# Kernel optimization log

Measured on AMD Instinct MI355X. Metric: run time of the kernel, lower is better.

The kernel has to match this reference:

```python
import jax, jax.numpy as jnp
import numpy as np

N, E, C, H, G, NC = 100000, 1600000, 128, 128, 256, 10
NEG_SLOPE = 0.2


def setup_inputs() -> dict:
    key = jax.random.key(0)
    ks = jax.random.split(key, 12)
    return {
        "x": jax.random.normal(ks[0], (N, C), jnp.float32),
        "edge_index": jax.random.randint(ks[1], (2, E), 0, N),
        "edge_attr": jax.random.uniform(ks[2], (E,), jnp.float32),
        "batch": jnp.sort(jax.random.randint(ks[3], (N,), 0, G)),
        "num_graphs": G,
        "att": jax.random.normal(ks[4], (3, 2 * C), jnp.float32) * (6.0 / (1 + 2 * C)) ** 0.5,
        "W1": jax.random.normal(ks[5], (3, C, H), jnp.float32) * (1.0 / C) ** 0.5,
        "b1": jnp.zeros((3, H), jnp.float32),
        "W2": jax.random.normal(ks[6], (3, H, H), jnp.float32) * (1.0 / H) ** 0.5,
        "b2": jnp.zeros((3, H), jnp.float32),
        "fc1_w": jax.random.normal(ks[7], (6 * H, 2 * H), jnp.float32) * (1.0 / (6 * H)) ** 0.5,
        "fc1_b": jnp.zeros((2 * H,), jnp.float32),
        "fc2_w": jax.random.normal(ks[8], (2 * H, H), jnp.float32) * (1.0 / (2 * H)) ** 0.5,
        "fc2_b": jnp.zeros((H,), jnp.float32),
        "fc3_w": jax.random.normal(ks[9], (H, NC), jnp.float32) * (1.0 / H) ** 0.5,
        "fc3_b": jnp.zeros((NC,), jnp.float32),
    }


def segment_sparsemax(z, seg, num_segments):
    """Exact sparsemax within each segment (ragged), vectorized via lexsort."""
    n = z.shape[0]
    order = jnp.lexsort((-z, seg))          # by segment asc, value desc
    zs, ss = z[order], seg[order]
    counts = jax.ops.segment_sum(jnp.ones((n,), jnp.int32), seg, num_segments)
    starts = jnp.cumsum(counts) - counts    # exclusive prefix -> segment start
    pos = jnp.arange(n, dtype=jnp.int32) - starts[ss]   # 0-based rank in segment
    ecs = jnp.cumsum(zs)
    base = jnp.concatenate([jnp.zeros((1,), zs.dtype), ecs])[starts[ss]]
    segcum = ecs - base                     # inclusive within-segment cumsum
    cond = 1.0 + (pos + 1).astype(zs.dtype) * zs > segcum  # support prefix mask
    k = jax.ops.segment_sum(cond.astype(zs.dtype), ss, num_segments)
    sum_k = jax.ops.segment_sum(jnp.where(cond, zs, 0.0), ss, num_segments)
    tau = jnp.where(k > 0, (sum_k - 1.0) / jnp.maximum(k, 1.0), 0.0)
    return jnp.maximum(z - tau[seg], 0.0)


def gcn_conv(x, row, col, ew, W, b, n_nodes):
    """PyG GCNConv with edge weights + self-loops (fill value 1)."""
    h = x @ W                                            # [N, H]
    deg = jax.ops.segment_sum(ew, col, n_nodes) + 1.0    # self-loop weight 1
    dinv = jnp.where(deg > 0, jax.lax.rsqrt(deg), 0.0)
    norm = dinv[row] * ew * dinv[col]                    # per-edge norm
    out = jax.ops.segment_sum(norm[:, None] * h[row], col, n_nodes)
    out = out + h * (dinv * dinv)[:, None]               # self-loop contribution
    return out + b


def emodel_block(x, row, col, att_b, W1_b, b1_b, W2_b, b2_b, n_nodes):
    # Edgelayer: att * cat([x[row], x[col]]) summed -> leaky_relu -> sparsemax(row)
    c = x.shape[1]
    s1 = x @ att_b[:c]                                   # [N]
    s2 = x @ att_b[c:]
    w = s1[row] + s2[col]
    w = jnp.where(w >= 0, w, NEG_SLOPE * w)              # leaky_relu
    p = segment_sparsemax(w, row, n_nodes)               # zero weight == pruned edge
    h = jax.nn.relu(gcn_conv(x, row, col, p, W1_b, b1_b, n_nodes))
    h = jax.nn.relu(gcn_conv(h, row, col, p, W2_b, b2_b, n_nodes))
    return h


def global_pools(z, batch, num_graphs):
    cnt = jax.ops.segment_sum(jnp.ones((z.shape[0], 1), z.dtype), batch, num_graphs)
    mean = jax.ops.segment_sum(z, batch, num_graphs) / jnp.maximum(cnt, 1.0)
    mx = jax.ops.segment_max(z, batch, num_graphs)
    mx = jnp.where(jnp.isfinite(mx), mx, 0.0)            # guard empty graphs
    return mean, mx


def reference(x, edge_index, edge_attr, batch, num_graphs, att, W1, b1, W2, b2,
              fc1_w, fc1_b, fc2_w, fc2_b, fc3_w, fc3_b):
    n_nodes = x.shape[0]
    row, col = edge_index[0], edge_index[1]
    feats = []
    for i in range(3):  # three structurally identical blocks with distinct params
        z = emodel_block(x, row, col, att[i], W1[i], b1[i], W2[i], b2[i], n_nodes)
        mean, mx = global_pools(z, batch, num_graphs)
        feats += [mean, mx]
    h = jnp.concatenate(feats, axis=1)                   # [G, 6*H]
    h = jax.nn.relu(h @ fc1_w + fc1_b)
    h = jax.nn.relu(h @ fc2_w + fc2_b)
    return jax.nn.log_softmax(h @ fc3_w + fc3_b, axis=-1)
```

## Files before the change

kernel.cpp:

```cpp
#include <hip/hip_runtime.h>
#include <math.h>

constexpr int NN   = 100000;
constexpr int EE   = 1600000;
constexpr int CH   = 128;
constexpr int GG   = 256;
constexpr int NCLS = 10;
constexpr int SW   = 48;
constexpr int QW   = 24;

constexpr int NB   = (NN + 63) >> 6;
constexpr int BCAP = 1344;
constexpr int EPT  = 8;
constexpr int BINTB = 256;
constexpr int EPB  = BINTB * EPT;

typedef _Float16 half8  __attribute__((ext_vector_type(8)));
typedef _Float16 half2v __attribute__((ext_vector_type(2)));
typedef float    float4v __attribute__((ext_vector_type(4)));

__global__ void bounds_kernel(const int* __restrict__ batch, int* __restrict__ gb,
                              int* __restrict__ bcur) {
    int t = blockIdx.x * blockDim.x + threadIdx.x;
    if (t < NB) bcur[t] = 0;
    if (t > GG) return;
    int lo = 0, hi = NN;
    while (lo < hi) {
        int mid = (lo + hi) >> 1;
        if (batch[mid] < t) lo = mid + 1; else hi = mid;
    }
    gb[t] = lo;
}

__global__ void wt16_kernel(const float* __restrict__ W1, const float* __restrict__ W2,
                            _Float16* __restrict__ wt) {
    int mat = blockIdx.x;
    const float* src = (mat < 3) ? (W1 + (size_t)mat * 16384)
                                 : (W2 + (size_t)(mat - 3) * 16384);
    _Float16* dst = wt + (size_t)mat * 16384;
    for (int i = threadIdx.x; i < 16384; i += 256) {
        int n = i >> 7, k = i & 127;
        dst[n * 128 + k] = (_Float16)src[k * 128 + n];
    }
}

__global__ void scores3_kernel(const float* __restrict__ x, const float* __restrict__ att,
                               float* __restrict__ s1, float* __restrict__ s2,
                               int* __restrict__ cur, _Float16* __restrict__ x16) {
    int wid  = threadIdx.x >> 6;
    int lane = threadIdx.x & 63;
    int node = blockIdx.x * 4 + wid;
    if (node >= NN) return;
    float x0 = x[node * CH + lane];
    float x1 = x[node * CH + 64 + lane];
    x16[(size_t)node * CH + lane]      = (_Float16)x0;
    x16[(size_t)node * CH + 64 + lane] = (_Float16)x1;
#pragma unroll
    for (int i = 0; i < 3; ++i) {
        const float* a = att + i * 256;
        float p1 = x0 * a[lane]       + x1 * a[64 + lane];
        float p2 = x0 * a[128 + lane] + x1 * a[192 + lane];
#pragma unroll
        for (int off = 32; off > 0; off >>= 1) {
            p1 += __shfl_xor(p1, off, 64);
            p2 += __shfl_xor(p2, off, 64);
        }
        if (lane == 0) { s1[i * NN + node] = p1; s2[i * NN + node] = p2; }
    }
    if (lane == 0) {
        cur[node]          = 0;
        cur[NN + node]     = 0;
        cur[2 * NN + node] = 0;
    }
}

__global__ __launch_bounds__(256) void bin_kernel(const int* __restrict__ ei,
                                                  int* __restrict__ bcur,
                                                  unsigned int* __restrict__ binned) {
    __shared__ int hist[NB];
    __shared__ int basearr[NB];
    int tid = threadIdx.x;
    for (int b = tid; b < NB; b += BINTB) hist[b] = 0;
    __syncthreads();
    int e0 = blockIdx.x * EPB;
    int r[EPT], c[EPT], off[EPT];
#pragma unroll
    for (int j = 0; j < EPT; ++j) {
        int e = e0 + j * BINTB + tid;
        if (e < EE) {
            r[j] = ei[e];
            c[j] = ei[EE + e];
            off[j] = atomicAdd(&hist[r[j] >> 6], 1);
        } else r[j] = -1;
    }
    __syncthreads();
    for (int b = tid; b < NB; b += BINTB) {
        int n = hist[b];
        basearr[b] = n ? atomicAdd(&bcur[b], n) : 0;
    }
    __syncthreads();
#pragma unroll
    for (int j = 0; j < EPT; ++j) {
        if (r[j] >= 0) {
            int b = r[j] >> 6;
            int pos = basearr[b] + off[j];
            if (pos < BCAP)
                binned[(size_t)b * BCAP + pos] = (unsigned)(r[j] & 63) | ((unsigned)c[j] << 6);
        }
    }
}

__global__ __launch_bounds__(1024) void buildtau_kernel(const int* __restrict__ bcur,
                                                        const unsigned int* __restrict__ binned,
                                                        const float* __restrict__ s1,
                                                        const float* __restrict__ s2,
                                                        float* __restrict__ taubuf) {
    __shared__ int slot[64 * SW];
    __shared__ int cntl[64];
    int b   = blockIdx.x;
    int tid = threadIdx.x;
    if (tid < 64) cntl[tid] = 0;
    __syncthreads();
    int cnt = min(bcur[b], BCAP);
    for (int idx = tid; idx < cnt; idx += 1024) {
        unsigned u = binned[(size_t)b * BCAP + idx];
        int rlo = u & 63;
        int p = atomicAdd(&cntl[rlo], 1);
        if (p < SW) slot[rlo * SW + p] = (int)(u >> 6);
    }
    __syncthreads();
    int wid  = tid >> 6, lane = tid & 63;
    int half = lane >> 5, l32 = lane & 31;
    const float NEGINF = __int_as_float(0xff800000);
    for (int pp = 0; pp < 2; ++pp) {
        int pb = wid * 4 + pp * 2;
        int v0 = (b << 6) + pb;
        if (v0 >= NN) break;
        int d0 = min(cntl[pb], SW), d1 = min(cntl[pb + 1], SW);
        if ((d0 | d1) == 0) continue;
        if (d0 <= 32 && d1 <= 32) {
            int mydeg = half ? d1 : d0;
            int myrlo = pb + half;
            int vv    = v0 + half;
            int c = (l32 < mydeg) ? slot[myrlo * SW + l32] : 0;
            float z[3];
#pragma unroll
            for (int i = 0; i < 3; ++i) {
                z[i] = NEGINF;
                if (l32 < mydeg) {
                    float w = s1[i * NN + vv] + s2[i * NN + c];
                    z[i] = (w >= 0.f) ? w : 0.2f * w;
                }
            }
#pragma unroll
            for (int k = 2; k <= 32; k <<= 1) {
#pragma unroll
                for (int j = k >> 1; j > 0; j >>= 1) {
                    bool keepMax = ((l32 & j) == 0) == ((l32 & k) == 0);
#pragma unroll
                    for (int i = 0; i < 3; ++i) {
                        float other = __shfl_xor(z[i], j, 64);
                        z[i] = keepMax ? fmaxf(z[i], other) : fminf(z[i], other);
                    }
                }
            }
            float cs[3];
#pragma unroll
            for (int i = 0; i < 3; ++i) cs[i] = z[i];
#pragma unroll
            for (int off = 1; off < 32; off <<= 1) {
#pragma unroll
                for (int i = 0; i < 3; ++i) {
                    float t = __shfl_up(cs[i], off, 64);
                    if (l32 >= off) cs[i] += t;
                }
            }
#pragma unroll
            for (int i = 0; i < 3; ++i) {
                bool cond = (l32 < mydeg) && (1.f + (float)(l32 + 1) * z[i] > cs[i]);
                unsigned long long m = __ballot(cond);
                int myk = half ? __popcll(m >> 32) : __popcll(m & 0xFFFFFFFFull);
                float sumk = __shfl(cs[i], half * 32 + max(myk, 1) - 1, 64);
                if (l32 == 0 && mydeg > 0)
                    taubuf[i * NN + vv] = (sumk - 1.f) / (float)max(myk, 1);
            }
        } else {
            for (int h = 0; h < 2; ++h) {
                int deg = h ? d1 : d0;
                if (deg == 0) continue;
                int rlo = pb + h;
                int v   = v0 + h;
                int c = (lane < deg) ? slot[rlo * SW + lane] : 0;
#pragma unroll
                for (int i = 0; i < 3; ++i) {
                    float z = NEGINF;
                    if (lane < deg) {
                        float w = s1[i * NN + v] + s2[i * NN + c];
                        z = (w >= 0.f) ? w : 0.2f * w;
                    }
#pragma unroll
                    for (int k = 2; k <= 64; k <<= 1) {
#pragma unroll
                        for (int j = k >> 1; j > 0; j >>= 1) {
                            float other = __shfl_xor(z, j, 64);
                            bool keepMax = ((lane & j) == 0) == ((lane & k) == 0);
                            z = keepMax ? fmaxf(z, other) : fminf(z, other);
                        }
                    }
                    float cs = z;
#pragma unroll
                    for (int off = 1; off < 64; off <<= 1) {
                        float t = __shfl_up(cs, off, 64);
                        if (lane >= off) cs += t;
                    }
                    bool cond = (lane < deg) && (1.f + (float)(lane + 1) * z > cs);
                    unsigned long long mask = __ballot(cond);
                    int k = __popcll(mask);
                    float sumk = __shfl(cs, k - 1, 64);
                    if (lane == 0) taubuf[i * NN + v] = (sumk - 1.f) / (float)k;
                }
            }
        }
    }
}

__global__ void compact_kernel(const int* __restrict__ ei, const float* __restrict__ s1,
                               const float* __restrict__ s2, const float* __restrict__ taubuf,
                               int* __restrict__ qcnt, int2* __restrict__ qslot) {
    int e = blockIdx.x * blockDim.x + threadIdx.x;
    if (e >= EE) return;
    int r = ei[e], c = ei[EE + e];
    float w = s1[r] + s2[c];
    w = (w >= 0.f) ? w : 0.2f * w;
    float p = w - taubuf[r];
    if (p > 0.f) {
        int pos = atomicAdd(&qcnt[c], 1);
        if (pos < QW) qslot[c * QW + pos] = make_int2(r, __float_as_int(p));
    }
}

__global__ void degq_kernel(const int* __restrict__ qcnt, const int2* __restrict__ qslot,
                            float* __restrict__ dinv) {
    int v = blockIdx.x * blockDim.x + threadIdx.x;
    if (v >= NN) return;
    int cnt = min(qcnt[v], QW);
    double d = 1.0;
    int base = v * QW;
    for (int t = 0; t < cnt; ++t) d += (double)__int_as_float(qslot[base + t].y);
    dinv[v] = rsqrtf((float)d);
}

__global__ __launch_bounds__(256) void gemm16_kernel(const _Float16* __restrict__ A,
                                                     const _Float16* __restrict__ WT,
                                                     _Float16* __restrict__ Cout, int M) {
    int lane = threadIdx.x & 63;
    int wid  = threadIdx.x >> 6;
    int l15  = lane & 15;
    int quad = lane >> 4;
    int rowbase = blockIdx.x * 64 + wid * 16;
    int arow = rowbase + l15;

    float4v acc[8];
#pragma unroll
    for (int n = 0; n < 8; ++n) acc[n] = (float4v){0.f, 0.f, 0.f, 0.f};

#pragma unroll
    for (int kc = 0; kc < 4; ++kc) {
        half8 a = {};
        if (arow < M) a = *(const half8*)(A + (size_t)arow * CH + kc * 32 + quad * 8);
#pragma unroll
        for (int n = 0; n < 8; ++n) {
            half8 b = *(const half8*)(WT + (size_t)(n * 16 + l15) * CH + kc * 32 + quad * 8);
            acc[n] = __builtin_amdgcn_mfma_f32_16x16x32_f16(a, b, acc[n], 0, 0, 0);
        }
    }
#pragma unroll
    for (int n = 0; n < 8; ++n) {
#pragma unroll
        for (int r = 0; r < 4; ++r) {
            int row = rowbase + quad * 4 + r;
            if (row < M) Cout[(size_t)row * CH + n * 16 + l15] = (_Float16)acc[n][r];
        }
    }
}

template <int OUTMODE>
__global__ void agg_kernel(const _Float16* __restrict__ hin,
                           const int* __restrict__ qcnt, const int2* __restrict__ qslot,
                           const float* __restrict__ dinv, const float* __restrict__ bias,
                           void* __restrict__ outv) {
    int wid  = threadIdx.x >> 6;
    int lane = threadIdx.x & 63;
    int v = blockIdx.x * 4 + wid;
    if (v >= NN) return;
    const half2v* hin2 = (const half2v*)hin;
    int cnt  = min(qcnt[v], QW);
    int base = v * QW;
    float dv = dinv[v];
    double ax = 0.0, ay = 0.0;
    if (cnt > 0 && cnt <= 6) {
        int2   ep_[6];
        float  g_[6];
        half2v hr_[6];
#pragma unroll
        for (int t = 0; t < 6; ++t) ep_[t] = qslot[base + min(t, cnt - 1)];
#pragma unroll
        for (int t = 0; t < 6; ++t) {
            g_[t]  = (t < cnt) ? __int_as_float(ep_[t].y) * dinv[ep_[t].x] : 0.f;
            hr_[t] = hin2[(size_t)ep_[t].x * 64 + lane];
        }
#pragma unroll
        for (int t = 0; t < 6; ++t) {
            ax += (double)g_[t] * (double)(float)hr_[t].x;
            ay += (double)g_[t] * (double)(float)hr_[t].y;
        }
    } else {
        for (int t = 0; t < cnt; ++t) {
            int2 ep = qslot[base + t];
            int r = ep.x;
            float g = __int_as_float(ep.y) * dinv[r];
            half2v hr = hin2[(size_t)r * 64 + lane];
            ax += (double)g * (double)(float)hr.x;
            ay += (double)g * (double)(float)hr.y;
        }
    }
    half2v hv = hin2[(size_t)v * 64 + lane];
    float2 b2 = ((const float2*)bias)[lane];
    float ox = fmaxf(dv * (float)ax + dv * dv * (float)hv.x + b2.x, 0.f);
    float oy = fmaxf(dv * (float)ay + dv * dv * (float)hv.y + b2.y, 0.f);
    if (OUTMODE == 0) {
        half2v o; o.x = (_Float16)ox; o.y = (_Float16)oy;
        ((half2v*)outv)[(size_t)v * 64 + lane] = o;
    } else {
        float2 o; o.x = ox; o.y = oy;
        ((float2*)outv)[(size_t)v * 64 + lane] = o;
    }
}

__global__ void pool_kernel(const float* __restrict__ z, const int* __restrict__ gb,
                            float* __restrict__ feats, int blk) {
    int g = blockIdx.x;
    int f = threadIdx.x;
    int s = gb[g], e = gb[g + 1];
    float sum = 0.f, mx = 0.f;
    const float* zp = z + (size_t)s * CH + f;
    int n = s;
    for (; n + 16 <= e; n += 16) {
        float v[16];
#pragma unroll
        for (int j = 0; j < 16; ++j) v[j] = zp[(size_t)j * CH];
#pragma unroll
        for (int j = 0; j < 16; ++j) {
            sum += v[j];
            mx = fmaxf(mx, v[j]);
        }
        zp += (size_t)16 * CH;
    }
    for (; n < e; ++n) {
        float v = *zp;
        sum += v;
        mx = fmaxf(mx, v);
        zp += CH;
    }
    int cnt = e - s;
    feats[g * 768 + blk * 256 + f]       = sum / (float)max(cnt, 1);
    feats[g * 768 + blk * 256 + 128 + f] = mx;
}

__global__ void fc1_kernel(const float* __restrict__ feats, const float* __restrict__ w,
                           const float* __restrict__ b, float* __restrict__ t1) {
    __shared__ float lf[768];
    int g = blockIdx.x, j = threadIdx.x;
    for (int i = j; i < 768; i += 256) lf[i] = feats[g * 768 + i];
    __syncthreads();
    float acc = b[j];
    for (int k = 0; k < 768; ++k) acc += lf[k] * w[k * 256 + j];
    t1[g * 256 + j] = fmaxf(acc, 0.f);
}

__global__ void fc23_kernel(const float* __restrict__ t1,
                            const float* __restrict__ w2, const float* __restrict__ b2,
                            const float* __restrict__ w3, const float* __restrict__ b3,
                            float* __restrict__ out) {
    __shared__ float lt[256];
    __shared__ float lh[128];
    __shared__ float lg[NCLS];
    int g = blockIdx.x, j = threadIdx.x;
    lt[j]       = t1[g * 256 + j];
    lt[j + 128] = t1[g * 256 + 128 + j];
    __syncthreads();
    float acc = b2[j];
    for (int k = 0; k < 256; ++k) acc += lt[k] * w2[k * 128 + j];
    lh[j] = fmaxf(acc, 0.f);
    __syncthreads();
    if (j < NCLS) {
        float a = b3[j];
        for (int k = 0; k < 128; ++k) a += lh[k] * w3[k * NCLS + j];
        lg[j] = a;
    }
    __syncthreads();
    if (j == 0) {
        float mxv = lg[0];
        for (int i = 1; i < NCLS; ++i) mxv = fmaxf(mxv, lg[i]);
        float se = 0.f;
        for (int i = 0; i < NCLS; ++i) se += expf(lg[i] - mxv);
        float lse = logf(se) + mxv;
        for (int i = 0; i < NCLS; ++i) out[g * NCLS + i] = lg[i] - lse;
    }
}

extern "C" void kernel_launch(void* const* d_in, const int* in_sizes, int n_in,
                              void* d_out, int out_size, void* d_ws, size_t ws_size,
                              hipStream_t stream) {
    const float* x     = (const float*)d_in[0];
    const int*   ei    = (const int*)  d_in[1];
    const int*   batch = (const int*)  d_in[3];
    const float* att   = (const float*)d_in[5];
    const float* W1    = (const float*)d_in[6];
    const float* b1    = (const float*)d_in[7];
    const float* W2    = (const float*)d_in[8];
    const float* b2    = (const float*)d_in[9];
    const float* fc1w  = (const float*)d_in[10];
    const float* fc1b  = (const float*)d_in[11];
    const float* fc2w  = (const float*)d_in[12];
    const float* fc2b  = (const float*)d_in[13];
    const float* fc3w  = (const float*)d_in[14];
    const float* fc3b  = (const float*)d_in[15];
    float* out = (float*)d_out;

    char* p = (char*)d_ws;
    auto carve = [&](size_t bytes) -> void* {
        void* r = (void*)p;
        p += (bytes + 255) & ~(size_t)255;
        return r;
    };
    int* cur  = (int*)carve((size_t)3 * NN * 4);
    int* qcnt = cur;
    void* adj = carve((size_t)NN * QW * 8);
    unsigned int* binned = (unsigned int*)adj;
    int2*         qslot  = (int2*)adj;
    int* gb   = (int*)carve((size_t)(GG + 1) * 4);
    int* bcur = (int*)carve((size_t)NB * 4);
    float* s1     = (float*)carve((size_t)3 * NN * 4);
    float* s2     = (float*)carve((size_t)3 * NN * 4);
    float* taubuf = (float*)carve((size_t)3 * NN * 4);
    float* dinv   = (float*)carve((size_t)NN * 4);
    _Float16* wt16 = (_Float16*)carve((size_t)6 * 16384 * 2);
    _Float16* x16  = (_Float16*)carve((size_t)NN * CH * 2);
    _Float16* bufA = (_Float16*)carve((size_t)NN * CH * 2);
    float* zbuf = (float*)carve((size_t)NN * CH * 4);
    _Float16* bufB = (_Float16*)zbuf;
    float* feats  = (float*)carve((size_t)GG * 768 * 4);
    float* t1     = (float*)carve((size_t)GG * 256 * 4);

    const int TB = 256;
    dim3 egrid((EE + TB - 1) / TB);
    dim3 ngrid((NN + TB - 1) / TB);
    dim3 wgrid((NN + 3) / 4);
    dim3 ggrid((NN + 63) / 64);
    dim3 bingrid((EE + EPB - 1) / EPB);
    dim3 bgrid((NB + TB - 1) / TB);

    scores3_kernel<<<wgrid, 256, 0, stream>>>(x, att, s1, s2, cur, x16);
    bounds_kernel<<<bgrid, TB, 0, stream>>>(batch, gb, bcur);
    bin_kernel<<<bingrid, BINTB, 0, stream>>>(ei, bcur, binned);
    wt16_kernel<<<6, 256, 0, stream>>>(W1, W2, wt16);
    buildtau_kernel<<<NB, 1024, 0, stream>>>(bcur, binned, s1, s2, taubuf);

    for (int i = 0; i < 3; ++i) {
        const float* s1_i  = s1 + (size_t)i * NN;
        const float* s2_i  = s2 + (size_t)i * NN;
        const float* tau_i = taubuf + (size_t)i * NN;
        int*         qc_i  = qcnt + (size_t)i * NN;
        const _Float16* WT1_i = wt16 + (size_t)i * 16384;
        const _Float16* WT2_i = wt16 + (size_t)(3 + i) * 16384;
        const float* b1_i  = b1 + i * CH;
        const float* b2_i  = b2 + i * CH;

        compact_kernel<<<egrid, TB, 0, stream>>>(ei, s1_i, s2_i, tau_i, qc_i, qslot);
        degq_kernel<<<ngrid, TB, 0, stream>>>(qc_i, qslot, dinv);

        gemm16_kernel<<<ggrid, 256, 0, stream>>>(x16, WT1_i, bufA, NN);
        agg_kernel<0><<<wgrid, 256, 0, stream>>>(bufA, qc_i, qslot, dinv, b1_i, bufB);
        gemm16_kernel<<<ggrid, 256, 0, stream>>>(bufB, WT2_i, bufA, NN);
        agg_kernel<1><<<wgrid, 256, 0, stream>>>(bufA, qc_i, qslot, dinv, b2_i, zbuf);

        pool_kernel<<<GG, 128, 0, stream>>>(zbuf, gb, feats, i);
    }

    fc1_kernel<<<GG, 256, 0, stream>>>(feats, fc1w, fc1b, t1);
    fc23_kernel<<<GG, 128, 0, stream>>>(t1, fc2w, fc2b, fc3w, fc3b, out);
}
```

Measured before the change: 987.4 us.

## Bucket nodes by degree in buildtau and pack small-degree nodes four per wave

The sparsemax tau kernel now sorts each bin's 64 nodes into three degree classes (up to 16, up to 32, larger) in shared memory. It processes four low-degree nodes per wavefront with 16-lane sorts, two mid-degree nodes per wave, and one high-degree node per wave, and it launches 512 threads per block instead of 1024. This is meant to cut wasted lanes and shuffle stages for the common low-degree case (average degree is about 16). The aggregation kernel's unrolled six-edge fast path is also removed in favour of the plain loop, which may lose memory-level parallelism for low-count nodes.

```diff
diff --git a/kernel.cpp b/kernel.cpp
--- a/kernel.cpp
+++ b/kernel.cpp
@@ -110,38 +110,99 @@
     }
 }
 
-__global__ __launch_bounds__(1024) void buildtau_kernel(const int* __restrict__ bcur,
-                                                        const unsigned int* __restrict__ binned,
-                                                        const float* __restrict__ s1,
-                                                        const float* __restrict__ s2,
-                                                        float* __restrict__ taubuf) {
+__global__ __launch_bounds__(512) void buildtau_kernel(const int* __restrict__ bcur,
+                                                       const unsigned int* __restrict__ binned,
+                                                       const float* __restrict__ s1,
+                                                       const float* __restrict__ s2,
+                                                       float* __restrict__ taubuf) {
     __shared__ int slot[64 * SW];
     __shared__ int cntl[64];
+    __shared__ int listA[64], listB[64], listC[64];
+    __shared__ int nA, nB, nC;
     int b   = blockIdx.x;
     int tid = threadIdx.x;
     if (tid < 64) cntl[tid] = 0;
+    if (tid == 0) { nA = 0; nB = 0; nC = 0; }
     __syncthreads();
     int cnt = min(bcur[b], BCAP);
-    for (int idx = tid; idx < cnt; idx += 1024) {
+    for (int idx = tid; idx < cnt; idx += 512) {
         unsigned u = binned[(size_t)b * BCAP + idx];
         int rlo = u & 63;
         int p = atomicAdd(&cntl[rlo], 1);
         if (p < SW) slot[rlo * SW + p] = (int)(u >> 6);
     }
     __syncthreads();
-    int wid  = tid >> 6, lane = tid & 63;
-    int half = lane >> 5, l32 = lane & 31;
+    if (tid < 64) {
+        int d = min(cntl[tid], SW);
+        if (d > 0) {
+            if (d <= 16)      listA[atomicAdd(&nA, 1)] = tid;
+            else if (d <= 32) listB[atomicAdd(&nB, 1)] = tid;
+            else              listC[atomicAdd(&nC, 1)] = tid;
+        }
+    }
+    __syncthreads();
+    int wid = tid >> 6, lane = tid & 63;
     const float NEGINF = __int_as_float(0xff800000);
-    for (int pp = 0; pp < 2; ++pp) {
-        int pb = wid * 4 + pp * 2;
-        int v0 = (b << 6) + pb;
-        if (v0 >= NN) break;
-        int d0 = min(cntl[pb], SW), d1 = min(cntl[pb + 1], SW);
-        if ((d0 | d1) == 0) continue;
-        if (d0 <= 32 && d1 <= 32) {
-            int mydeg = half ? d1 : d0;
-            int myrlo = pb + half;
-            int vv    = v0 + half;
+
+    {
+        int grp = lane >> 4, l16 = lane & 15;
+        for (int ia = wid * 4; ia < nA; ia += 32) {
+            int idx   = min(ia + grp, nA - 1);
+            int myrlo = listA[idx];
+            int mydeg = (ia + grp < nA) ? min(cntl[myrlo], SW) : 0;
+            int vv    = (b << 6) + myrlo;
+            int c = (l16 < mydeg) ? slot[myrlo * SW + l16] : 0;
+            float z[3];
+#pragma unroll
+            for (int i = 0; i < 3; ++i) {
+                z[i] = NEGINF;
+                if (l16 < mydeg) {
+                    float w = s1[i * NN + vv] + s2[i * NN + c];
+                    z[i] = (w >= 0.f) ? w : 0.2f * w;
+                }
+            }
+#pragma unroll
+            for (int k = 2; k <= 16; k <<= 1) {
+#pragma unroll
+                for (int j = k >> 1; j > 0; j >>= 1) {
+                    bool keepMax = ((l16 & j) == 0) == ((l16 & k) == 0);
+#pragma unroll
+                    for (int i = 0; i < 3; ++i) {
+                        float other = __shfl_xor(z[i], j, 64);
+                        z[i] = keepMax ? fmaxf(z[i], other) : fminf(z[i], other);
+                    }
+                }
+            }
+            float cs[3];
+#pragma unroll
+            for (int i = 0; i < 3; ++i) cs[i] = z[i];
+#pragma unroll
+            for (int off = 1; off < 16; off <<= 1) {
+#pragma unroll
+                for (int i = 0; i < 3; ++i) {
+                    float t = __shfl_up(cs[i], off, 64);
+                    if (l16 >= off) cs[i] += t;
+                }
+            }
+#pragma unroll
+            for (int i = 0; i < 3; ++i) {
+                bool cond = (l16 < mydeg) && (1.f + (float)(l16 + 1) * z[i] > cs[i]);
+                unsigned long long m = __ballot(cond);
+                int myk = __popcll((m >> (grp * 16)) & 0xFFFFull);
+                float sumk = __shfl(cs[i], grp * 16 + max(myk, 1) - 1, 64);
+                if (l16 == 0 && mydeg > 0)
+                    taubuf[i * NN + vv] = (sumk - 1.f) / (float)max(myk, 1);
+            }
+        }
+    }
+
+    {
+        int half = lane >> 5, l32 = lane & 31;
+        for (int ib = wid * 2; ib < nB; ib += 16) {
+            int idx   = min(ib + half, nB - 1);
+            int myrlo = listB[idx];
+            int mydeg = (ib + half < nB) ? min(cntl[myrlo], SW) : 0;
+            int vv    = (b << 6) + myrlo;
             int c = (l32 < mydeg) ? slot[myrlo * SW + l32] : 0;
             float z[3];
 #pragma unroll
@@ -184,42 +245,41 @@
                 if (l32 == 0 && mydeg > 0)
                     taubuf[i * NN + vv] = (sumk - 1.f) / (float)max(myk, 1);
             }
-        } else {
-            for (int h = 0; h < 2; ++h) {
-                int deg = h ? d1 : d0;
-                if (deg == 0) continue;
-                int rlo = pb + h;
-                int v   = v0 + h;
-                int c = (lane < deg) ? slot[rlo * SW + lane] : 0;
-#pragma unroll
-                for (int i = 0; i < 3; ++i) {
-                    float z = NEGINF;
-                    if (lane < deg) {
-                        float w = s1[i * NN + v] + s2[i * NN + c];
-                        z = (w >= 0.f) ? w : 0.2f * w;
-                    }
-#pragma unroll
-                    for (int k = 2; k <= 64; k <<= 1) {
-#pragma unroll
-                        for (int j = k >> 1; j > 0; j >>= 1) {
-                            float other = __shfl_xor(z, j, 64);
-                            bool keepMax = ((lane & j) == 0) == ((lane & k) == 0);
-                            z = keepMax ? fmaxf(z, other) : fminf(z, other);
-                        }
-                    }
-                    float cs = z;
-#pragma unroll
-                    for (int off = 1; off < 64; off <<= 1) {
-                        float t = __shfl_up(cs, off, 64);
-                        if (lane >= off) cs += t;
-                    }
-                    bool cond = (lane < deg) && (1.f + (float)(lane + 1) * z > cs);
-                    unsigned long long mask = __ballot(cond);
-                    int k = __popcll(mask);
-                    float sumk = __shfl(cs, k - 1, 64);
-                    if (lane == 0) taubuf[i * NN + v] = (sumk - 1.f) / (float)k;
-                }
-            }
+        }
+    }
+
+    for (int ic = wid; ic < nC; ic += 8) {
+        int rlo = listC[ic];
+        int deg = min(cntl[rlo], SW);
+        int v   = (b << 6) + rlo;
+        int c = (lane < deg) ? slot[rlo * SW + lane] : 0;
+#pragma unroll
+        for (int i = 0; i < 3; ++i) {
+            float z = NEGINF;
+            if (lane < deg) {
+                float w = s1[i * NN + v] + s2[i * NN + c];
+                z = (w >= 0.f) ? w : 0.2f * w;
+            }
+#pragma unroll
+            for (int k = 2; k <= 64; k <<= 1) {
+#pragma unroll
+                for (int j = k >> 1; j > 0; j >>= 1) {
+                    float other = __shfl_xor(z, j, 64);
+                    bool keepMax = ((lane & j) == 0) == ((lane & k) == 0);
+                    z = keepMax ? fmaxf(z, other) : fminf(z, other);
+                }
+            }
+            float cs = z;
+#pragma unroll
+            for (int off = 1; off < 64; off <<= 1) {
+                float t = __shfl_up(cs, off, 64);
+                if (lane >= off) cs += t;
+            }
+            bool cond = (lane < deg) && (1.f + (float)(lane + 1) * z > cs);
+            unsigned long long mask = __ballot(cond);
+            int k = __popcll(mask);
+            float sumk = __shfl(cs, k - 1, 64);
+            if (lane == 0) taubuf[i * NN + v] = (sumk - 1.f) / (float)k;
         }
     }
 }
@@ -298,31 +358,13 @@
     int base = v * QW;
     float dv = dinv[v];
     double ax = 0.0, ay = 0.0;
-    if (cnt > 0 && cnt <= 6) {
-        int2   ep_[6];
-        float  g_[6];
-        half2v hr_[6];
-#pragma unroll
-        for (int t = 0; t < 6; ++t) ep_[t] = qslot[base + min(t, cnt - 1)];
-#pragma unroll
-        for (int t = 0; t < 6; ++t) {
-            g_[t]  = (t < cnt) ? __int_as_float(ep_[t].y) * dinv[ep_[t].x] : 0.f;
-            hr_[t] = hin2[(size_t)ep_[t].x * 64 + lane];
-        }
-#pragma unroll
-        for (int t = 0; t < 6; ++t) {
-            ax += (double)g_[t] * (double)(float)hr_[t].x;
-            ay += (double)g_[t] * (double)(float)hr_[t].y;
-        }
-    } else {
-        for (int t = 0; t < cnt; ++t) {
-            int2 ep = qslot[base + t];
-            int r = ep.x;
-            float g = __int_as_float(ep.y) * dinv[r];
-            half2v hr = hin2[(size_t)r * 64 + lane];
-            ax += (double)g * (double)(float)hr.x;
-            ay += (double)g * (double)(float)hr.y;
-        }
+    for (int t = 0; t < cnt; ++t) {
+        int2 ep = qslot[base + t];
+        int r = ep.x;
+        float g = __int_as_float(ep.y) * dinv[r];
+        half2v hr = hin2[(size_t)r * 64 + lane];
+        ax += (double)g * (double)(float)hr.x;
+        ay += (double)g * (double)(float)hr.y;
     }
     half2v hv = hin2[(size_t)v * 64 + lane];
     float2 b2 = ((const float2*)bias)[lane];
@@ -465,7 +507,7 @@
     bounds_kernel<<<bgrid, TB, 0, stream>>>(batch, gb, bcur);
     bin_kernel<<<bingrid, BINTB, 0, stream>>>(ei, bcur, binned);
     wt16_kernel<<<6, 256, 0, stream>>>(W1, W2, wt16);
-    buildtau_kernel<<<NB, 1024, 0, stream>>>(bcur, binned, s1, s2, taubuf);
+    buildtau_kernel<<<NB, 512, 0, stream>>>(bcur, binned, s1, s2, taubuf);
 
     for (int i = 0; i < 3; ++i) {
         const float* s1_i  = s1 + (size_t)i * NN;
```

New measurement: 954.8 us. 1.03x faster.
